# Performance work log

Measured on AMD Instinct MI355X. Metric: run time of the kernel, lower is better.

Reference implementation:

```python
import jax, jax.numpy as jnp
import numpy as np

N = 50000          # site nodes
L = 32             # max URL token length
E = 64             # embed_size
H = 128            # hidden_size
E_SIM = 800000     # edges per relation in blocks
E_SUB = 200000     # 'sim' edges classified at the end
NEG = 0.01         # LeakyReLU negative slope

def leaky(x):
    return jnp.where(x >= 0, x, NEG * x)

def lstm_final(x, mask, Wih, Whh, b, reverse):
    # x: [N, L, E], mask: [N, L] bool. Returns packed-sequence final hidden [N, E].
    if reverse:
        x = x[:, ::-1, :]
        mask = mask[:, ::-1]
    h0 = jnp.zeros((x.shape[0], Whh.shape[1]), x.dtype)
    def step(carry, inp):
        h, c = carry
        xt, mt = inp
        g = xt @ Wih.T + h @ Whh.T + b
        i, f, gg, o = jnp.split(g, 4, axis=-1)  # PyTorch gate order i,f,g,o
        cn = jax.nn.sigmoid(f) * c + jax.nn.sigmoid(i) * jnp.tanh(gg)
        hn = jax.nn.sigmoid(o) * jnp.tanh(cn)
        m = mt[:, None]
        return (jnp.where(m, hn, h), jnp.where(m, cn, c)), None
    (h, _), _ = jax.lax.scan(step, (h0, h0), (x.transpose(1, 0, 2), mask.T))
    return h

def graph_conv(h, src, dst, W, b):
    # DGL GraphConv, norm='both': D_dst^{-1/2} A D_src^{-1/2} h W + b  (degrees clamped to >=1)
    n = h.shape[0]
    ones = jnp.ones(src.shape[0], h.dtype)
    out_deg = jnp.clip(jax.ops.segment_sum(ones, src, num_segments=n), 1.0)
    in_deg = jnp.clip(jax.ops.segment_sum(ones, dst, num_segments=n), 1.0)
    feat = h * jax.lax.rsqrt(out_deg)[:, None]
    if W.shape[0] > W.shape[1]:
        feat = feat @ W  # project before gather/scatter when in_dim > out_dim (as DGL does)
        rst = jax.ops.segment_sum(feat[src], dst, num_segments=n)
    else:
        rst = jax.ops.segment_sum(feat[src], dst, num_segments=n) @ W
    return rst * jax.lax.rsqrt(in_deg)[:, None] + b

def setup_inputs():
    key = jax.random.key(0)
    ks = iter(jax.random.split(key, 64))
    def nrm(shape, scale=0.05):
        return jax.random.normal(next(ks), shape, dtype=jnp.float32) * scale
    inp = {}
    inp["inputs_s"] = jax.random.randint(next(ks), (N, L), 0, 128)
    lengths = jax.random.randint(next(ks), (N,), 1, L + 1)
    inp["inputs_sm"] = (jnp.arange(L)[None, :] < lengths[:, None]).astype(jnp.int32)
    inp["inputs_c"] = jax.random.randint(next(ks), (N, 1), 0, 101)
    inp["inputs_co"] = jax.random.randint(next(ks), (N, 1), 0, 92)
    inp["inputs_sl"] = jax.random.randint(next(ks), (N, 1), 0, 6)
    for name, m in [("sim_src", E_SIM), ("sim_dst", E_SIM), ("user_src", E_SIM),
                    ("user_dst", E_SIM), ("esub_src", E_SUB), ("esub_dst", E_SUB)]:
        inp[name] = jax.random.randint(next(ks), (m,), 0, N)
    inp["emb_url"] = nrm((128, E)); inp["emb_cat"] = nrm((101, E))
    inp["emb_country"] = nrm((92, E)); inp["emb_sl"] = nrm((6, E))
    for d in ("f", "b"):
        inp["Wih_" + d] = nrm((4 * E, E)); inp["Whh_" + d] = nrm((4 * E, E))
        inp["b_" + d] = nrm((4 * E,))  # b_ih + b_hh folded into one bias
    inp["fc_W"] = nrm((E, 2 * E)); inp["fc_b"] = nrm((E,))
    for i, din in enumerate([4 * E, H]):
        for rel in ("sim", "user"):
            inp["gcn%d_%s_W" % (i, rel)] = nrm((din, H))
            inp["gcn%d_%s_b" % (i, rel)] = nrm((H,))
    inp["cls_W1"] = nrm((H, 2 * H)); inp["cls_b1"] = nrm((H,))
    inp["bn_g"] = jnp.ones((H,), jnp.float32); inp["bn_b"] = jnp.zeros((H,), jnp.float32)
    inp["cls_W2"] = nrm((2, H)); inp["cls_b2"] = nrm((2,))
    return inp

def reference(inputs_s, inputs_sm, inputs_c, inputs_co, inputs_sl,
              sim_src, sim_dst, user_src, user_dst, esub_src, esub_dst,
              emb_url, emb_cat, emb_country, emb_sl,
              Wih_f, Whh_f, b_f, Wih_b, Whh_b, b_b, fc_W, fc_b,
              gcn0_sim_W, gcn0_sim_b, gcn0_user_W, gcn0_user_b,
              gcn1_sim_W, gcn1_sim_b, gcn1_user_W, gcn1_user_b,
              cls_W1, cls_b1, bn_g, bn_b, cls_W2, cls_b2):
    mask = inputs_sm.astype(bool)
    x = emb_url[inputs_s]                                # [N, L, E]
    hf = lstm_final(x, mask, Wih_f, Whh_f, b_f, False)   # h_n[0]
    hb = lstm_final(x, mask, Wih_b, Whh_b, b_b, True)    # h_n[1]
    h_url = leaky(jnp.concatenate([hf, hb], -1) @ fc_W.T + fc_b)  # dropout = identity (eval)
    h = jnp.concatenate([h_url, emb_cat[inputs_c[:, 0]],
                         emb_country[inputs_co[:, 0]], emb_sl[inputs_sl[:, 0]]], -1)  # [N, 4E]
    layers = [(gcn0_sim_W, gcn0_sim_b, gcn0_user_W, gcn0_user_b),
              (gcn1_sim_W, gcn1_sim_b, gcn1_user_W, gcn1_user_b)]
    for Ws, bs, Wu, bu in layers:  # HeteroGraphConv aggregate='sum'
        h = leaky(graph_conv(h, sim_src, sim_dst, Ws, bs)
                  + graph_conv(h, user_src, user_dst, Wu, bu))
    feat = jnp.concatenate([h[esub_src], h[esub_dst]], -1)  # [E_SUB, 2H]
    z = feat @ cls_W1.T + cls_b1
    z = (z - z.mean(0)) * jax.lax.rsqrt(z.var(0) + 1e-5) * bn_g + bn_b  # BatchNorm1d (batch stats)
    z = jnp.maximum(z, 0.0)
    return z @ cls_W2.T + cls_b2
```

## Files before the change

### kernel.cpp

```cpp
#include <hip/hip_runtime.h>
#include <hip/hip_bf16.h>
#include <stdint.h>

#define N_NODES 50000
#define SEQ_L   32
#define NE_BIG  800000
#define NE_SUB  200000
#define DSTRIDE 64

typedef __hip_bfloat16 bf16;
typedef unsigned short u16;
typedef _Float16 f16;
typedef _Float16 v8h __attribute__((ext_vector_type(8)));
typedef float v4f __attribute__((ext_vector_type(4)));

__device__ __forceinline__ float b2f(bf16 x) { return __bfloat162float(x); }
__device__ __forceinline__ float leakyf(float v) { return v >= 0.f ? v : 0.01f * v; }
__device__ __forceinline__ u16 f2h_bits(float x) { f16 h = (f16)x; u16 b; __builtin_memcpy(&b, &h, 2); return b; }
__device__ __forceinline__ float h2f(u16 b) { f16 h; __builtin_memcpy(&h, &b, 2); return (float)h; }
__device__ __forceinline__ uint pack2h(float a, float b) { return (uint)f2h_bits(a) | ((uint)f2h_bits(b) << 16); }

__device__ __forceinline__ float ldf(const void* p, int i, int isbf) {
  return isbf ? b2f(((const bf16*)p)[i]) : ((const float*)p)[i];
}

__device__ __forceinline__ int detect_isbf(const u16* __restrict__ u) {
  __shared__ int insane;
  if (threadIdx.x == 0) insane = 0;
  __syncthreads();
  int expo = (u[threadIdx.x * 2] >> 7) & 0xFF;
  if (expo >= 147) atomicAdd(&insane, 1);
  __syncthreads();
  return insane == 0;
}

struct PrepArgs {
  const void* Whh_f; const void* Whh_b; const void* fc_W; const void* cls_W1;
  const void* g0sW; const void* g0uW; const void* g1sW; const void* g1uW;
  const void* emb_cat; const void* emb_country; const void* emb_sl;
  const void* fc_b; const void* cls_b1; const void* g0sb; const void* g0ub;
  const void* g1sb; const void* g1ub; const void* bn_g; const void* bn_b;
  const void* cls_W2; const void* cls_b2;
  const void* emb_url; const void* Wih_f; const void* b_f; const void* Wih_b; const void* b_b;
  f16* Whh_h; u16* Bfc; u16* BW1; u16* Bg0; u16* Bg1;
  u16* embc_h; u16* embco_h; u16* embs_h;
  float* fcb; float* b1; float* g0sbP; float* g0ubP; float* g1sbP; float* g1ubP;
  float* bngP; float* bnbP; float* W2P; float* b2P;
  int* dflag;
  float* Xperm;
  const int* sm; int* lens; int* cnt33;
  const int* s0; const int* d0; const int* s1; const int* d1;
  int* cnt4; int* col0; int* col1;
};

__global__ __launch_bounds__(256) void prep_graph_kernel(PrepArgs A) {
  const int b = blockIdx.x;
  const int t = threadIdx.x;
  const int NBL = (N_NODES + 255) / 256;
  const int NBE = (NE_BIG + 255) / 256;

  if (b >= 1186) {
    int rel = (b - 1186) / NBE;
    int e = ((b - 1186) % NBE) * 256 + t;
    if (e >= NE_BIG) return;
    const int* s = rel ? A.s1 : A.s0;
    const int* d = rel ? A.d1 : A.d0;
    int* col = rel ? A.col1 : A.col0;
    int* base = A.cnt4 + (size_t)rel * 2 * N_NODES;
    int sv = s[e], dv = d[e];
    atomicAdd(&base[sv], 1);
    int p = atomicAdd(&base[N_NODES + dv], 1);
    if (p < DSTRIDE) col[(size_t)dv * DSTRIDE + p] = sv;
    return;
  }
  if (b >= 990) {
    int i = (b - 990) * 256 + t;
    if (i >= N_NODES) return;
    int len = 0;
#pragma unroll
    for (int tt = 0; tt < SEQ_L; ++tt) len += A.sm[i * SEQ_L + tt];
    A.lens[i] = len;
    atomicAdd(&A.cnt33[len], 1);
    return;
  }

  const int isbf = detect_isbf((const u16*)A.emb_url);
  auto cpy = [&](const void* s, float* d, int n, int boff) {
    int i = (b - boff) * 256 + t;
    if (i < n) d[i] = ldf(s, i, isbf);
  };
  auto cvh = [&](const void* s, u16* d, int n, int boff) {
    int i = (b - boff) * 256 + t;
    if (i < n) d[i] = f2h_bits(ldf(s, i, isbf));
  };
  auto trh = [&](const void* s, u16* d, int R, int C, int KOFF, int boff) {
    int i = (b - boff) * 256 + t;
    if (i < R * C) { int r = i / C, c = i % C; d[c * 256 + KOFF + r] = f2h_bits(ldf(s, i, isbf)); }
  };
  if      (b <   64) cvh(A.Whh_f, (u16*)A.Whh_h, 16384, 0);
  else if (b <  128) cvh(A.Whh_b, (u16*)(A.Whh_h + 16384), 16384, 64);
  else if (b <  160) cvh(A.fc_W, A.Bfc, 8192, 128);
  else if (b <  288) cvh(A.cls_W1, A.BW1, 32768, 160);
  else if (b <  416) trh(A.g0sW, A.Bg0, 256, 128, 0, 288);
  else if (b <  544) trh(A.g0uW, A.Bg0 + 128 * 256, 256, 128, 0, 416);
  else if (b <  608) trh(A.g1sW, A.Bg1, 128, 128, 0, 544);
  else if (b <  672) trh(A.g1uW, A.Bg1, 128, 128, 128, 608);
  else if (b <  698) cvh(A.emb_cat, A.embc_h, 6464, 672);
  else if (b <  721) cvh(A.emb_country, A.embco_h, 5888, 698);
  else if (b <  723) cvh(A.emb_sl, A.embs_h, 384, 721);
  else if (b <  724) cpy(A.fc_b, A.fcb, 64, 723);
  else if (b <  725) cpy(A.cls_b1, A.b1, 128, 724);
  else if (b <  726) cpy(A.g0sb, A.g0sbP, 128, 725);
  else if (b <  727) cpy(A.g0ub, A.g0ubP, 128, 726);
  else if (b <  728) cpy(A.g1sb, A.g1sbP, 128, 727);
  else if (b <  729) cpy(A.g1ub, A.g1ubP, 128, 728);
  else if (b <  730) cpy(A.bn_g, A.bngP, 128, 729);
  else if (b <  731) cpy(A.bn_b, A.bnbP, 128, 730);
  else if (b <  732) cpy(A.cls_W2, A.W2P, 256, 731);
  else if (b <  733) { cpy(A.cls_b2, A.b2P, 2, 732); if (t == 0) A.dflag[0] = isbf; }
  else if (b <  989) {
    int bb = b - 733;
    int dir = bb >> 7;
    int v = bb & 127;
    const void* Wih = dir ? A.Wih_b : A.Wih_f;
    const void* bias = dir ? A.b_b : A.b_f;
    __shared__ float embL[64];
    if (t < 64) embL[t] = ldf(A.emb_url, v * 64 + t, isbf);
    __syncthreads();
    float acc = ldf(bias, t, isbf);
#pragma unroll 8
    for (int j = 0; j < 64; ++j) acc += embL[j] * ldf(Wih, t * 64 + j, isbf);
    int g = t >> 6, unit = t & 63;
    A.Xperm[(size_t)dir * 128 * 256 + v * 256 + unit * 4 + g] = acc;
  }
}
#define PG_BLOCKS (1186 + 2 * 3125)

__global__ __launch_bounds__(256) void permfill_rsq_kernel(
    const int* __restrict__ lens, const int* __restrict__ cnt33, int* __restrict__ cur33,
    int* __restrict__ perm,
    const int* __restrict__ cnt4, float* __restrict__ rsq4)
{
  const int b = blockIdx.x, t = threadIdx.x;
  const int NBL = (N_NODES + 255) / 256;
  if (b < NBL) {
    int i = b * 256 + t;
    if (i >= N_NODES) return;
    int len = lens[i];
    int base = 0;
    for (int l = len + 1; l <= SEQ_L; ++l) base += cnt33[l];
    int p = atomicAdd(&cur33[len], 1);
    perm[base + p] = i;
  } else {
    int i = (b - NBL) * 256 + t;
    if (i >= 4 * N_NODES) return;
    int c = cnt4[i]; if (c < 1) c = 1;
    rsq4[i] = __builtin_amdgcn_rsqf((float)c);
  }
}
#define PR_BLOCKS (196 + 782)

__global__ __launch_bounds__(256, 4) void lstm_mfma_kernel(
    const int* __restrict__ perm, const int* __restrict__ lens,
    const int* __restrict__ toksg,
    const float* __restrict__ Xperm,
    const f16* __restrict__ Whh_h,
    u16* __restrict__ hcat_h,
    int nnodes)
{
  __shared__ __align__(16) f16 H[2][64 * 72];
  __shared__ int toksL[2][64];
  __shared__ int permL[64];
  __shared__ int lensL[64];
  __shared__ int smax;
  const int tid = threadIdx.x;
  const int w = tid >> 6;
  const int lane = tid & 63;
  const int quad = lane >> 4;
  const int lid = lane & 15;
  const int dir = blockIdx.y;

  if (tid < 64) {
    int gid = blockIdx.x * 64 + tid;
    int node = -1, len = 0;
    if (gid < nnodes) { node = perm[gid]; len = lens[node]; }
    permL[tid] = node; lensL[tid] = len;
  }
  if (tid == 0) smax = 0;
  for (int i = tid; i < 64 * 72; i += 256) { H[0][i] = (f16)0.f; H[1][i] = (f16)0.f; }
  __syncthreads();
  if (tid < 64 && lensL[tid] > 0) atomicMax(&smax, lensL[tid]);
  __syncthreads();
  const int tmax = smax;

  const f16* Wd = Whh_h + (size_t)dir * 256 * 64;
  v8h Bf[4][2];
#pragma unroll
  for (int g = 0; g < 4; ++g)
#pragma unroll
    for (int kf = 0; kf < 2; ++kf)
      Bf[g][kf] = *(const v8h*)(Wd + (g * 64 + w * 16 + lid) * 64 + kf * 32 + quad * 8);

  int lenv[16];
#pragma unroll
  for (int mt = 0; mt < 4; ++mt)
#pragma unroll
    for (int r = 0; r < 4; ++r) lenv[mt * 4 + r] = lensL[mt * 16 + quad * 4 + r];

  float creg[16];
  f16 hreg[16];
#pragma unroll
  for (int i = 0; i < 16; ++i) { creg[i] = 0.f; hreg[i] = (f16)0.f; }

  const float* Xp = Xperm + (size_t)dir * 128 * 256;

  if (tid < 64) {
    int len = lensL[tid];
    int tok = 0;
    if (len > 0) tok = toksg[(size_t)permL[tid] * SEQ_L + (dir ? (len - 1) : 0)];
    toksL[0][tid] = tok;
  }
  __syncthreads();

  for (int step = 0; step < tmax; ++step) {
    const int rb = step & 1, wb = rb ^ 1;
#pragma unroll
    for (int mt = 0; mt < 4; ++mt) {
      float4 xr[4];
#pragma unroll
      for (int r = 0; r < 4; ++r) {
        int nd = mt * 16 + quad * 4 + r;
        xr[r] = *(const float4*)(Xp + (size_t)toksL[rb][nd] * 256 + (w * 16 + lid) * 4);
      }
      const f16* hb = &H[rb][0];
      int arow = (mt * 16 + lid) * 72 + quad * 8;
      v8h a0 = *(const v8h*)(hb + arow);
      v8h a1 = *(const v8h*)(hb + arow + 32);
      v4f acc[4];
#pragma unroll
      for (int g = 0; g < 4; ++g) {
        v4f a = {0.f, 0.f, 0.f, 0.f};
        a = __builtin_amdgcn_mfma_f32_16x16x32_f16(a0, Bf[g][0], a, 0, 0, 0);
        a = __builtin_amdgcn_mfma_f32_16x16x32_f16(a1, Bf[g][1], a, 0, 0, 0);
        acc[g] = a;
      }
#pragma unroll
      for (int r = 0; r < 4; ++r) {
        int idx = mt * 4 + r;
        int nd = mt * 16 + quad * 4 + r;
        bool act = step < lenv[idx];
        float gi = acc[0][r] + xr[r].x;
        float gf = acc[1][r] + xr[r].y;
        float gG = acc[2][r] + xr[r].z;
        float go = acc[3][r] + xr[r].w;
        float A = __expf(-gi);
        float B = __expf(-gf);
        float C = __expf(-go);
        float D = __expf(2.f * fminf(gG, 15.f));
        float sf = __builtin_amdgcn_rcpf(1.f + B);
        float sitg = (D - 1.f) * __builtin_amdgcn_rcpf((1.f + A) * (D + 1.f));
        float cn = sf * creg[idx] + sitg;
        float E = __expf(2.f * fminf(cn, 15.f));
        float hn = (E - 1.f) * __builtin_amdgcn_rcpf((1.f + C) * (E + 1.f));
        if (act) { creg[idx] = cn; hreg[idx] = (f16)hn; }
        H[wb][nd * 72 + w * 16 + lid] = hreg[idx];
      }
    }
    if (tid < 64 && step + 1 < tmax) {
      int len = lensL[tid];
      int tok = 0;
      if (step + 1 < len) {
        int t = dir ? (len - 2 - step) : (step + 1);
        tok = toksg[(size_t)permL[tid] * SEQ_L + t];
      }
      toksL[wb][tid] = tok;
    }
    __syncthreads();
  }
#pragma unroll
  for (int mt = 0; mt < 4; ++mt)
#pragma unroll
    for (int r = 0; r < 4; ++r) {
      int nd = mt * 16 + quad * 4 + r;
      int gnode = permL[nd];
      if (gnode >= 0) {
        u16 bits; f16 hv = hreg[mt * 4 + r]; __builtin_memcpy(&bits, &hv, 2);
        hcat_h[(size_t)gnode * 128 + dir * 64 + w * 16 + lid] = bits;
      }
    }
}

template<int K, int COLS, int AMODE, bool LEAKY, int OHS, bool EMB, bool BNS>
__global__ __launch_bounds__(256) void mfma_gemm(
    const u16* __restrict__ Ah,
    const int* __restrict__ esrc, const int* __restrict__ edst, const u16* __restrict__ Fh,
    const u16* __restrict__ B,
    const float* __restrict__ bias, const float* __restrict__ bias2,
    const float* __restrict__ rs0, const float* __restrict__ rs1,
    u16* __restrict__ outh0, u16* __restrict__ outh1,
    const int* __restrict__ ic, const int* __restrict__ ico, const int* __restrict__ isl,
    const u16* __restrict__ ech, const u16* __restrict__ ecoh, const u16* __restrict__ eslh,
    float* __restrict__ bnsums,
    int nrows)
{
  constexpr int AST = K + 8;
  constexpr int ABYTES = 64 * AST * 2;
  constexpr int EBYTES = 64 * 129 * 4;
  constexpr int SBYTES = (ABYTES > EBYTES) ? ABYTES : EBYTES;
  __shared__ __align__(16) char smem[SBYTES];
  u16* As = (u16*)smem;
  float* Es = (float*)smem;
  __shared__ int idxL[128];
  __shared__ float bnred[BNS ? 512 : 1];

  const int tid = threadIdx.x;
  const int w = tid >> 6;
  const int lane = tid & 63;
  const int quad = lane >> 4;
  const int lid = lane & 15;
  const int r0 = blockIdx.x * 64;

  if (AMODE == 2) {
    if (tid < 64) {
      int row = r0 + tid;
      idxL[tid] = (row < nrows) ? esrc[row] : -1;
      idxL[64 + tid] = (row < nrows) ? edst[row] : -1;
    }
    __syncthreads();
    for (int idx = tid; idx < 64 * (K / 8); idx += 256) {
      int rn = idx / (K / 8), seg = idx % (K / 8);
      int half = seg >> 4, k8 = seg & 15;
      int base = idxL[half * 64 + rn];
      uint4 v = {0u, 0u, 0u, 0u};
      if (base >= 0) v = *(const uint4*)(Fh + (size_t)base * 128 + k8 * 8);
      *(uint4*)(As + rn * AST + seg * 8) = v;
    }
  } else {
    for (int idx = tid; idx < 64 * (K / 8); idx += 256) {
      int rn = idx / (K / 8), c8 = idx % (K / 8);
      int row = r0 + rn;
      uint4 v = {0u, 0u, 0u, 0u};
      if (row < nrows) v = *(const uint4*)(Ah + (size_t)row * K + c8 * 8);
      *(uint4*)(As + rn * AST + c8 * 8) = v;
    }
  }
  __syncthreads();

  constexpr int NT = COLS / 16;
  v4f acc[NT];
#pragma unroll
  for (int i = 0; i < NT; ++i) acc[i] = (v4f){0.f, 0.f, 0.f, 0.f};

  for (int kb = 0; kb < K / 32; ++kb) {
    v8h a = *(const v8h*)((const f16*)As + (w * 16 + lid) * AST + kb * 32 + quad * 8);
#pragma unroll
    for (int ct = 0; ct < NT; ++ct) {
      v8h b = *(const v8h*)((const f16*)B + (size_t)(ct * 16 + lid) * K + kb * 32 + quad * 8);
      acc[ct] = __builtin_amdgcn_mfma_f32_16x16x32_f16(a, b, acc[ct], 0, 0, 0);
    }
  }

  constexpr int NH = (COLS > 128) ? 2 : 1;
  constexpr int CH = COLS / NH;
  float bs = 0.f, bs2 = 0.f;
#pragma unroll
  for (int h = 0; h < NH; ++h) {
    __syncthreads();
#pragma unroll
    for (int ct = 0; ct < CH / 16; ++ct) {
      int ctg = h * (CH / 16) + ct;
#pragma unroll
      for (int r = 0; r < 4; ++r)
        Es[(w * 16 + quad * 4 + r) * 129 + ct * 16 + lid] = acc[ctg][r];
    }
    __syncthreads();
    for (int idx = tid; idx < 64 * CH; idx += 256) {
      int rn = idx / CH, c = idx % CH;
      int row = r0 + rn;
      float v = 0.f;
      if (row < nrows) {
        v = Es[rn * 129 + c];
        if (bias) v += bias[h * CH + c];
        if (bias2) v += bias2[h * CH + c];
        if (LEAKY) v = leakyf(v);
        const float* rs = (h == 0) ? rs0 : rs1;
        if (rs) v *= rs[row];
        u16* oh = (h == 0) ? outh0 : outh1;
        oh[(size_t)row * OHS + c] = f2h_bits(v);
      }
      if (BNS) { bs += v; bs2 += v * v; }
    }
  }
  if (BNS) {
    bnred[tid] = bs;
    bnred[256 + tid] = bs2;
    __syncthreads();
    if (tid < 128) {
      atomicAdd(&bnsums[tid], bnred[tid] + bnred[tid + 128]);
      atomicAdd(&bnsums[128 + tid], bnred[256 + tid] + bnred[384 + tid]);
    }
  }
  if (EMB) {
    for (int idx = tid; idx < 64 * 192; idx += 256) {
      int rn = idx / 192, j = idx % 192;
      int row = r0 + rn;
      if (row >= nrows) continue;
      u16 v;
      if (j < 64)       v = ech [ic [row] * 64 + j];
      else if (j < 128) v = ecoh[ico[row] * 64 + (j - 64)];
      else              v = eslh[isl[row] * 64 + (j - 128)];
      outh0[(size_t)row * OHS + 64 + j] = v;
    }
  }
}

__global__ __launch_bounds__(256) void gather_merge0_kernel(
    const int* __restrict__ colS, const int* __restrict__ cntS, const u16* __restrict__ Ps,
    const int* __restrict__ colU, const int* __restrict__ cntU, const u16* __restrict__ Pu,
    const float* __restrict__ rsS, const float* __restrict__ rsU,
    const float* __restrict__ bS, const float* __restrict__ bU,
    u16* __restrict__ outh, int nnodes)
{
  int wave = threadIdx.x >> 6;
  int lane = threadIdx.x & 63;
  int node = __builtin_amdgcn_readfirstlane(blockIdx.x * 4 + wave);
  if (node >= nnodes) return;
  const uint* PS2 = (const uint*)Ps;
  const uint* PU2 = (const uint*)Pu;
  float2 aS = make_float2(0.f, 0.f), aU = make_float2(0.f, 0.f);
  {
    const int* col = colS + (size_t)node * DSTRIDE;
    int cnt = min(cntS[node], DSTRIDE);
    int e = 0;
    for (; e + 4 <= cnt; e += 4) {
      uint v0 = PS2[(size_t)col[e] * 64 + lane];
      uint v1 = PS2[(size_t)col[e + 1] * 64 + lane];
      uint v2 = PS2[(size_t)col[e + 2] * 64 + lane];
      uint v3 = PS2[(size_t)col[e + 3] * 64 + lane];
      aS.x += h2f((u16)v0) + h2f((u16)v1) + h2f((u16)v2) + h2f((u16)v3);
      aS.y += h2f((u16)(v0 >> 16)) + h2f((u16)(v1 >> 16)) + h2f((u16)(v2 >> 16)) + h2f((u16)(v3 >> 16));
    }
    for (; e < cnt; ++e) {
      uint v = PS2[(size_t)col[e] * 64 + lane];
      aS.x += h2f((u16)v); aS.y += h2f((u16)(v >> 16));
    }
  }
  {
    const int* col = colU + (size_t)node * DSTRIDE;
    int cnt = min(cntU[node], DSTRIDE);
    int e = 0;
    for (; e + 4 <= cnt; e += 4) {
      uint v0 = PU2[(size_t)col[e] * 64 + lane];
      uint v1 = PU2[(size_t)col[e + 1] * 64 + lane];
      uint v2 = PU2[(size_t)col[e + 2] * 64 + lane];
      uint v3 = PU2[(size_t)col[e + 3] * 64 + lane];
      aU.x += h2f((u16)v0) + h2f((u16)v1) + h2f((u16)v2) + h2f((u16)v3);
      aU.y += h2f((u16)(v0 >> 16)) + h2f((u16)(v1 >> 16)) + h2f((u16)(v2 >> 16)) + h2f((u16)(v3 >> 16));
    }
    for (; e < cnt; ++e) {
      uint v = PU2[(size_t)col[e] * 64 + lane];
      aU.x += h2f((u16)v); aU.y += h2f((u16)(v >> 16));
    }
  }
  float rS = rsS[node], rU = rsU[node];
  float2 bsv = ((const float2*)bS)[lane];
  float2 buv = ((const float2*)bU)[lane];
  float o0 = leakyf(aS.x * rS + bsv.x + aU.x * rU + buv.x);
  float o1 = leakyf(aS.y * rS + bsv.y + aU.y * rU + buv.y);
  ((uint*)outh)[(size_t)node * 64 + lane] = pack2h(o0, o1);
}

__global__ __launch_bounds__(256) void gather_cat1_kernel(
    const int* __restrict__ colS, const int* __restrict__ cntS,
    const int* __restrict__ colU, const int* __restrict__ cntU,
    const u16* __restrict__ Fh,
    const float* __restrict__ rsoutS, const float* __restrict__ rsoutU,
    const float* __restrict__ rsinS, const float* __restrict__ rsinU,
    u16* __restrict__ Acat, int nnodes)
{
  int wave = threadIdx.x >> 6;
  int lane = threadIdx.x & 63;
  int node = __builtin_amdgcn_readfirstlane(blockIdx.x * 4 + wave);
  if (node >= nnodes) return;
  const uint* F2 = (const uint*)Fh;
  float2 aS = make_float2(0.f, 0.f), aU = make_float2(0.f, 0.f);
  {
    const int* col = colS + (size_t)node * DSTRIDE;
    int cnt = min(cntS[node], DSTRIDE);
    int e = 0;
    for (; e + 2 <= cnt; e += 2) {
      int s0 = col[e], s1 = col[e + 1];
      float c0 = rsoutS[s0], c1 = rsoutS[s1];
      uint v0 = F2[(size_t)s0 * 64 + lane];
      uint v1 = F2[(size_t)s1 * 64 + lane];
      aS.x += c0 * h2f((u16)v0) + c1 * h2f((u16)v1);
      aS.y += c0 * h2f((u16)(v0 >> 16)) + c1 * h2f((u16)(v1 >> 16));
    }
    for (; e < cnt; ++e) {
      int s = col[e]; float c = rsoutS[s];
      uint v = F2[(size_t)s * 64 + lane];
      aS.x += c * h2f((u16)v); aS.y += c * h2f((u16)(v >> 16));
    }
  }
  {
    const int* col = colU + (size_t)node * DSTRIDE;
    int cnt = min(cntU[node], DSTRIDE);
    int e = 0;
    for (; e + 2 <= cnt; e += 2) {
      int s0 = col[e], s1 = col[e + 1];
      float c0 = rsoutU[s0], c1 = rsoutU[s1];
      uint v0 = F2[(size_t)s0 * 64 + lane];
      uint v1 = F2[(size_t)s1 * 64 + lane];
      aU.x += c0 * h2f((u16)v0) + c1 * h2f((u16)v1);
      aU.y += c0 * h2f((u16)(v0 >> 16)) + c1 * h2f((u16)(v1 >> 16));
    }
    for (; e < cnt; ++e) {
      int s = col[e]; float c = rsoutU[s];
      uint v = F2[(size_t)s * 64 + lane];
      aU.x += c * h2f((u16)v); aU.y += c * h2f((u16)(v >> 16));
    }
  }
  float rs = rsinS[node], ru = rsinU[node];
  ((uint*)Acat)[(size_t)node * 128 + lane] = pack2h(aS.x * rs, aS.y * rs);
  ((uint*)Acat)[(size_t)node * 128 + 64 + lane] = pack2h(aU.x * ru, aU.y * ru);
}

__global__ __launch_bounds__(256) void out_kernel(
    const u16* __restrict__ zh, const float* __restrict__ bnsums,
    const float* __restrict__ g, const float* __restrict__ bb, float M,
    const float* __restrict__ W2, const float* __restrict__ b2,
    void* __restrict__ out, int Mi, const int* __restrict__ flag)
{
  __shared__ float lds[128 * 65];
  __shared__ float red[64 * 8];
  __shared__ float ssL[256];
  const int tid = threadIdx.x;
  const int n = tid & 63;
  const int q = __builtin_amdgcn_readfirstlane(tid >> 6);
  const int r0 = blockIdx.x * 64;
  if (tid < 128) {
    float mean = bnsums[tid] / M;
    float var = bnsums[128 + tid] / M - mean * mean;
    float sc = g[tid] * __builtin_amdgcn_rsqf(var + 1e-5f);
    ssL[tid] = sc;
    ssL[128 + tid] = bb[tid] - mean * sc;
  }
  for (int idx = tid; idx < 64 * 128; idx += 256) {
    int rn = idx >> 7, j = idx & 127;
    int row = r0 + rn;
    lds[j * 65 + rn] = (row < Mi) ? h2f(zh[(size_t)row * 128 + j]) : 0.f;
  }
  __syncthreads();
  float a0 = 0.f, a1 = 0.f;
#pragma unroll 8
  for (int jj = 0; jj < 32; ++jj) {
    int j = q * 32 + jj;
    float y = lds[j * 65 + n] * ssL[j] + ssL[128 + j];
    y = y > 0.f ? y : 0.f;
    a0 += y * W2[j];
    a1 += y * W2[128 + j];
  }
  red[n * 8 + q * 2 + 0] = a0;
  red[n * 8 + q * 2 + 1] = a1;
  __syncthreads();
  if (q == 0 && (r0 + n) < Mi) {
    float o0 = red[n * 8] + red[n * 8 + 2] + red[n * 8 + 4] + red[n * 8 + 6] + b2[0];
    float o1 = red[n * 8 + 1] + red[n * 8 + 3] + red[n * 8 + 5] + red[n * 8 + 7] + b2[1];
    size_t oi = (size_t)(r0 + n) * 2;
    if (*flag) {
      ((bf16*)out)[oi + 0] = __float2bfloat16(o0);
      ((bf16*)out)[oi + 1] = __float2bfloat16(o1);
    } else {
      ((float*)out)[oi + 0] = o0;
      ((float*)out)[oi + 1] = o1;
    }
  }
}

extern "C" void kernel_launch(void* const* d_in, const int* in_sizes, int n_in,
                              void* d_out, int out_size, void* d_ws, size_t ws_size,
                              hipStream_t stream) {
  (void)in_sizes; (void)n_in; (void)out_size; (void)ws_size;
  const int N = N_NODES;
  const int* inputs_s  = (const int*)d_in[0];
  const int* inputs_sm = (const int*)d_in[1];
  const int* inputs_c  = (const int*)d_in[2];
  const int* inputs_co = (const int*)d_in[3];
  const int* inputs_sl = (const int*)d_in[4];
  const int* sim_src   = (const int*)d_in[5];
  const int* sim_dst   = (const int*)d_in[6];
  const int* user_src  = (const int*)d_in[7];
  const int* user_dst  = (const int*)d_in[8];
  const int* esub_src  = (const int*)d_in[9];
  const int* esub_dst  = (const int*)d_in[10];

  char* base = (char*)d_ws;
  size_t off = 0;
  auto alloc = [&](size_t bytes) -> char* {
    char* p = base + off;
    off += (bytes + 255) & ~(size_t)255;
    return p;
  };
  int* dflag    = (int*)alloc(256);
  f16* Whh_h    = (f16*)alloc(2 * 256 * 64 * 2);
  float* Xperm  = (float*)alloc(2 * 128 * 256 * 4);
  u16* Bfc      = (u16*)alloc(64 * 128 * 2);
  u16* BW1      = (u16*)alloc(128 * 256 * 2);
  u16* Bg0      = (u16*)alloc(256 * 256 * 2);
  u16* Bg1      = (u16*)alloc(128 * 256 * 2);
  u16* P_embc_h = (u16*)alloc(6464 * 2);
  u16* P_embco_h= (u16*)alloc(5888 * 2);
  u16* P_embs_h = (u16*)alloc(384 * 2);
  float* P_fcb  = (float*)alloc(64 * 4);
  float* P_b1   = (float*)alloc(128 * 4);
  float* P_g0sb = (float*)alloc(128 * 4);
  float* P_g0ub = (float*)alloc(128 * 4);
  float* P_g1sb = (float*)alloc(128 * 4);
  float* P_g1ub = (float*)alloc(128 * 4);
  float* P_bng  = (float*)alloc(128 * 4);
  float* P_bnb  = (float*)alloc(128 * 4);
  float* P_W2   = (float*)alloc(256 * 4);
  float* P_b2   = (float*)alloc(2 * 4);
  int* lens     = (int*)alloc((size_t)N * 4);
  int* perm     = (int*)alloc((size_t)N * 4);
  float* rsq4   = (float*)alloc((size_t)4 * N * 4);
  char* zbase   = alloc((size_t)4 * N * 4 + 3 * 256 + 1024);
  int* cnt4     = (int*)zbase;
  int* cnt33    = (int*)(zbase + (size_t)4 * N * 4);
  int* cur33    = cnt33 + 64;
  float* bnsums = (float*)(zbase + (size_t)4 * N * 4 + 512);
  const size_t zbytes = (size_t)4 * N * 4 + 3 * 256 + 1024;
  char* bufA = alloc((size_t)N * 256 * 4);
  char* bufB = alloc((size_t)N * 256 * 2);
  char* bufC = alloc((size_t)N * 256 * 2);
  char* bufE = alloc((size_t)N * 128 * 2);
  u16* h_h     = (u16*)bufA;
  u16* zh      = (u16*)bufA;
  int* col_sim = (int*)(bufA + (size_t)N * 256 * 2);
  int* col_usr = (int*)(bufA + (size_t)N * 256 * 2 + (size_t)N * DSTRIDE * 4);
  u16* hcat_h = (u16*)bufB;
  u16* h1_h   = (u16*)bufB;
  u16* Ps_h   = (u16*)bufC;
  u16* Pu_h   = Ps_h + (size_t)N * 128;
  u16* Acat   = (u16*)bufC;
  u16* F_h    = (u16*)bufE;

  const int NB64 = (N + 63) / 64;
  const int NBZ  = (NE_SUB + 63) / 64;

  hipMemsetAsync(zbase, 0, zbytes, stream);

  PrepArgs PA;
  PA.Whh_f = d_in[16]; PA.Whh_b = d_in[19]; PA.fc_W = d_in[21]; PA.cls_W1 = d_in[31];
  PA.g0sW = d_in[23]; PA.g0uW = d_in[25]; PA.g1sW = d_in[27]; PA.g1uW = d_in[29];
  PA.emb_cat = d_in[12]; PA.emb_country = d_in[13]; PA.emb_sl = d_in[14];
  PA.fc_b = d_in[22]; PA.cls_b1 = d_in[32]; PA.g0sb = d_in[24]; PA.g0ub = d_in[26];
  PA.g1sb = d_in[28]; PA.g1ub = d_in[30]; PA.bn_g = d_in[33]; PA.bn_b = d_in[34];
  PA.cls_W2 = d_in[35]; PA.cls_b2 = d_in[36];
  PA.emb_url = d_in[11]; PA.Wih_f = d_in[15]; PA.b_f = d_in[17]; PA.Wih_b = d_in[18]; PA.b_b = d_in[20];
  PA.Whh_h = Whh_h; PA.Bfc = Bfc; PA.BW1 = BW1; PA.Bg0 = Bg0; PA.Bg1 = Bg1;
  PA.embc_h = P_embc_h; PA.embco_h = P_embco_h; PA.embs_h = P_embs_h;
  PA.fcb = P_fcb; PA.b1 = P_b1; PA.g0sbP = P_g0sb; PA.g0ubP = P_g0ub; PA.g1sbP = P_g1sb; PA.g1ubP = P_g1ub;
  PA.bngP = P_bng; PA.bnbP = P_bnb; PA.W2P = P_W2; PA.b2P = P_b2;
  PA.dflag = dflag; PA.Xperm = Xperm;
  PA.sm = inputs_sm; PA.lens = lens; PA.cnt33 = cnt33;
  PA.s0 = sim_src; PA.d0 = sim_dst; PA.s1 = user_src; PA.d1 = user_dst;
  PA.cnt4 = cnt4; PA.col0 = col_sim; PA.col1 = col_usr;
  prep_graph_kernel<<<PG_BLOCKS, 256, 0, stream>>>(PA);

  permfill_rsq_kernel<<<PR_BLOCKS, 256, 0, stream>>>(lens, cnt33, cur33, perm, cnt4, rsq4);

  lstm_mfma_kernel<<<dim3(NB64, 2), 256, 0, stream>>>(perm, lens, inputs_s, Xperm, Whh_h, hcat_h, N);

  mfma_gemm<128, 64, 1, true, 256, true, false><<<NB64, 256, 0, stream>>>(
      hcat_h, nullptr, nullptr, nullptr, Bfc, P_fcb, nullptr, nullptr, nullptr,
      h_h, nullptr, inputs_c, inputs_co, inputs_sl, P_embc_h, P_embco_h, P_embs_h, nullptr, N);

  mfma_gemm<256, 256, 1, false, 128, false, false><<<NB64, 256, 0, stream>>>(
      h_h, nullptr, nullptr, nullptr, Bg0, nullptr, nullptr, rsq4, rsq4 + 2 * N,
      Ps_h, Pu_h, nullptr, nullptr, nullptr, nullptr, nullptr, nullptr, nullptr, N);

  gather_merge0_kernel<<<(N + 3) / 4, 256, 0, stream>>>(col_sim, cnt4 + N, Ps_h,
                                                        col_usr, cnt4 + 3 * N, Pu_h,
                                                        rsq4 + N, rsq4 + 3 * N, P_g0sb, P_g0ub, h1_h, N);

  gather_cat1_kernel<<<(N + 3) / 4, 256, 0, stream>>>(col_sim, cnt4 + N, col_usr, cnt4 + 3 * N, h1_h,
                                                      rsq4, rsq4 + 2 * N, rsq4 + N, rsq4 + 3 * N, Acat, N);

  mfma_gemm<256, 128, 1, true, 128, false, false><<<NB64, 256, 0, stream>>>(
      Acat, nullptr, nullptr, nullptr, Bg1, P_g1sb, P_g1ub, nullptr, nullptr,
      F_h, nullptr, nullptr, nullptr, nullptr, nullptr, nullptr, nullptr, nullptr, N);

  mfma_gemm<256, 128, 2, false, 128, false, true><<<NBZ, 256, 0, stream>>>(
      nullptr, esub_src, esub_dst, F_h, BW1, P_b1, nullptr, nullptr, nullptr,
      zh, nullptr, nullptr, nullptr, nullptr, nullptr, nullptr, nullptr, bnsums, NE_SUB);

  out_kernel<<<NBZ, 256, 0, stream>>>(zh, bnsums, P_bng, P_bnb, (float)NE_SUB,
                                      P_W2, P_b2, d_out, NE_SUB, dflag);
}
```

Before: 1.128 ms.

## Overlap graph edge CSR build with LSTM blocks and shrink column indices

Moves the edge degree counting and adjacency-list build out of the prep kernel and into the LSTM launch, interleaving four edge blocks per LSTM block so latency-bound atomics run alongside the recurrent MFMA work. The rsqrt-degree computation moves into extra blocks of the first FC GEMM. Column indices are stored as 16-bit instead of 32-bit, halving the adjacency footprint that the gather kernels read. This relies on node ids fitting in 16 bits, which fails for 50000 > 32767? No, u16 holds up to 65535, so it fits. The mixed kernel, however, keeps the LSTM's shared memory and launch bounds on the edge blocks, which may limit occupancy for them.

```diff
diff --git a/kernel.cpp b/kernel.cpp
--- a/kernel.cpp
+++ b/kernel.cpp
@@ -49,30 +49,12 @@
   int* dflag;
   float* Xperm;
   const int* sm; int* lens; int* cnt33;
-  const int* s0; const int* d0; const int* s1; const int* d1;
-  int* cnt4; int* col0; int* col1;
 };
 
 __global__ __launch_bounds__(256) void prep_graph_kernel(PrepArgs A) {
   const int b = blockIdx.x;
   const int t = threadIdx.x;
-  const int NBL = (N_NODES + 255) / 256;
-  const int NBE = (NE_BIG + 255) / 256;
-
-  if (b >= 1186) {
-    int rel = (b - 1186) / NBE;
-    int e = ((b - 1186) % NBE) * 256 + t;
-    if (e >= NE_BIG) return;
-    const int* s = rel ? A.s1 : A.s0;
-    const int* d = rel ? A.d1 : A.d0;
-    int* col = rel ? A.col1 : A.col0;
-    int* base = A.cnt4 + (size_t)rel * 2 * N_NODES;
-    int sv = s[e], dv = d[e];
-    atomicAdd(&base[sv], 1);
-    int p = atomicAdd(&base[N_NODES + dv], 1);
-    if (p < DSTRIDE) col[(size_t)dv * DSTRIDE + p] = sv;
-    return;
-  }
+
   if (b >= 990) {
     int i = (b - 990) * 256 + t;
     if (i >= N_NODES) return;
@@ -134,54 +116,71 @@
     A.Xperm[(size_t)dir * 128 * 256 + v * 256 + unit * 4 + g] = acc;
   }
 }
-#define PG_BLOCKS (1186 + 2 * 3125)
-
-__global__ __launch_bounds__(256) void permfill_rsq_kernel(
+#define PG_BLOCKS 1186
+
+__global__ __launch_bounds__(256) void permfill_kernel(
     const int* __restrict__ lens, const int* __restrict__ cnt33, int* __restrict__ cur33,
-    int* __restrict__ perm,
-    const int* __restrict__ cnt4, float* __restrict__ rsq4)
+    int* __restrict__ perm)
 {
-  const int b = blockIdx.x, t = threadIdx.x;
-  const int NBL = (N_NODES + 255) / 256;
-  if (b < NBL) {
-    int i = b * 256 + t;
-    if (i >= N_NODES) return;
-    int len = lens[i];
-    int base = 0;
-    for (int l = len + 1; l <= SEQ_L; ++l) base += cnt33[l];
-    int p = atomicAdd(&cur33[len], 1);
-    perm[base + p] = i;
-  } else {
-    int i = (b - NBL) * 256 + t;
-    if (i >= 4 * N_NODES) return;
-    int c = cnt4[i]; if (c < 1) c = 1;
-    rsq4[i] = __builtin_amdgcn_rsqf((float)c);
-  }
-}
-#define PR_BLOCKS (196 + 782)
-
-__global__ __launch_bounds__(256, 4) void lstm_mfma_kernel(
+  int i = blockIdx.x * 256 + threadIdx.x;
+  if (i >= N_NODES) return;
+  int len = lens[i];
+  int base = 0;
+  for (int l = len + 1; l <= SEQ_L; ++l) base += cnt33[l];
+  int p = atomicAdd(&cur33[len], 1);
+  perm[base + p] = i;
+}
+#define PF_BLOCKS 196
+
+#define LSTM_BLOCKS 1564
+#define EDGE_BLOCKS 6250
+__global__ __launch_bounds__(256, 4) void lstm_edge_kernel(
     const int* __restrict__ perm, const int* __restrict__ lens,
     const int* __restrict__ toksg,
     const float* __restrict__ Xperm,
     const f16* __restrict__ Whh_h,
     u16* __restrict__ hcat_h,
+    const int* __restrict__ s0, const int* __restrict__ d0,
+    const int* __restrict__ s1, const int* __restrict__ d1,
+    int* __restrict__ cnt4, u16* __restrict__ col0, u16* __restrict__ col1,
     int nnodes)
 {
+  const int bid = blockIdx.x;
+  const int tid = threadIdx.x;
+
+  if (bid % 5 != 0) {
+    int eb = bid - 1 - bid / 5;
+    if (eb >= EDGE_BLOCKS) return;
+    int rel = eb / 3125;
+    int e = (eb % 3125) * 256 + tid;
+    if (e >= NE_BIG) return;
+    const int* s = rel ? s1 : s0;
+    const int* d = rel ? d1 : d0;
+    u16* col = rel ? col1 : col0;
+    int* basep = cnt4 + (size_t)rel * 2 * N_NODES;
+    int sv = s[e], dv = d[e];
+    atomicAdd(&basep[sv], 1);
+    int p = atomicAdd(&basep[N_NODES + dv], 1);
+    if (p < DSTRIDE) col[(size_t)dv * DSTRIDE + p] = (u16)sv;
+    return;
+  }
+
+  const int l = bid / 5;
+  const int dir = l / 782;
+  const int bx = l % 782;
+
   __shared__ __align__(16) f16 H[2][64 * 72];
   __shared__ int toksL[2][64];
   __shared__ int permL[64];
   __shared__ int lensL[64];
   __shared__ int smax;
-  const int tid = threadIdx.x;
   const int w = tid >> 6;
   const int lane = tid & 63;
   const int quad = lane >> 4;
   const int lid = lane & 15;
-  const int dir = blockIdx.y;
 
   if (tid < 64) {
-    int gid = blockIdx.x * 64 + tid;
+    int gid = bx * 64 + tid;
     int node = -1, len = 0;
     if (gid < nnodes) { node = perm[gid]; len = lens[node]; }
     permL[tid] = node; lensL[tid] = len;
@@ -290,7 +289,7 @@
     }
 }
 
-template<int K, int COLS, int AMODE, bool LEAKY, int OHS, bool EMB, bool BNS>
+template<int K, int COLS, int AMODE, bool LEAKY, int OHS, bool EMB, bool BNS, bool RSQT = false>
 __global__ __launch_bounds__(256) void mfma_gemm(
     const u16* __restrict__ Ah,
     const int* __restrict__ esrc, const int* __restrict__ edst, const u16* __restrict__ Fh,
@@ -301,8 +300,20 @@
     const int* __restrict__ ic, const int* __restrict__ ico, const int* __restrict__ isl,
     const u16* __restrict__ ech, const u16* __restrict__ ecoh, const u16* __restrict__ eslh,
     float* __restrict__ bnsums,
+    const int* __restrict__ cntin, float* __restrict__ rsqout,
     int nrows)
 {
+  if (RSQT) {
+    int nbm = (nrows + 63) >> 6;
+    if ((int)blockIdx.x >= nbm) {
+      int i = ((int)blockIdx.x - nbm) * 256 + (int)threadIdx.x;
+      if (i < 4 * N_NODES) {
+        int c = cntin[i]; if (c < 1) c = 1;
+        rsqout[i] = __builtin_amdgcn_rsqf((float)c);
+      }
+      return;
+    }
+  }
   constexpr int AST = K + 8;
   constexpr int ABYTES = 64 * AST * 2;
   constexpr int EBYTES = 64 * 129 * 4;
@@ -415,8 +426,8 @@
 }
 
 __global__ __launch_bounds__(256) void gather_merge0_kernel(
-    const int* __restrict__ colS, const int* __restrict__ cntS, const u16* __restrict__ Ps,
-    const int* __restrict__ colU, const int* __restrict__ cntU, const u16* __restrict__ Pu,
+    const u16* __restrict__ colS, const int* __restrict__ cntS, const u16* __restrict__ Ps,
+    const u16* __restrict__ colU, const int* __restrict__ cntU, const u16* __restrict__ Pu,
     const float* __restrict__ rsS, const float* __restrict__ rsU,
     const float* __restrict__ bS, const float* __restrict__ bU,
     u16* __restrict__ outh, int nnodes)
@@ -429,7 +440,7 @@
   const uint* PU2 = (const uint*)Pu;
   float2 aS = make_float2(0.f, 0.f), aU = make_float2(0.f, 0.f);
   {
-    const int* col = colS + (size_t)node * DSTRIDE;
+    const u16* col = colS + (size_t)node * DSTRIDE;
     int cnt = min(cntS[node], DSTRIDE);
     int e = 0;
     for (; e + 4 <= cnt; e += 4) {
@@ -446,7 +457,7 @@
     }
   }
   {
-    const int* col = colU + (size_t)node * DSTRIDE;
+    const u16* col = colU + (size_t)node * DSTRIDE;
     int cnt = min(cntU[node], DSTRIDE);
     int e = 0;
     for (; e + 4 <= cnt; e += 4) {
@@ -471,8 +482,8 @@
 }
 
 __global__ __launch_bounds__(256) void gather_cat1_kernel(
-    const int* __restrict__ colS, const int* __restrict__ cntS,
-    const int* __restrict__ colU, const int* __restrict__ cntU,
+    const u16* __restrict__ colS, const int* __restrict__ cntS,
+    const u16* __restrict__ colU, const int* __restrict__ cntU,
     const u16* __restrict__ Fh,
     const float* __restrict__ rsoutS, const float* __restrict__ rsoutU,
     const float* __restrict__ rsinS, const float* __restrict__ rsinU,
@@ -485,7 +496,7 @@
   const uint* F2 = (const uint*)Fh;
   float2 aS = make_float2(0.f, 0.f), aU = make_float2(0.f, 0.f);
   {
-    const int* col = colS + (size_t)node * DSTRIDE;
+    const u16* col = colS + (size_t)node * DSTRIDE;
     int cnt = min(cntS[node], DSTRIDE);
     int e = 0;
     for (; e + 2 <= cnt; e += 2) {
@@ -503,7 +514,7 @@
     }
   }
   {
-    const int* col = colU + (size_t)node * DSTRIDE;
+    const u16* col = colU + (size_t)node * DSTRIDE;
     int cnt = min(cntU[node], DSTRIDE);
     int e = 0;
     for (; e + 2 <= cnt; e += 2) {
@@ -636,8 +647,8 @@
   char* bufE = alloc((size_t)N * 128 * 2);
   u16* h_h     = (u16*)bufA;
   u16* zh      = (u16*)bufA;
-  int* col_sim = (int*)(bufA + (size_t)N * 256 * 2);
-  int* col_usr = (int*)(bufA + (size_t)N * 256 * 2 + (size_t)N * DSTRIDE * 4);
+  u16* col_sim = (u16*)(bufA + (size_t)N * 256 * 2);
+  u16* col_usr = (u16*)(bufA + (size_t)N * 256 * 2 + (size_t)N * DSTRIDE * 2);
   u16* hcat_h = (u16*)bufB;
   u16* h1_h   = (u16*)bufB;
   u16* Ps_h   = (u16*)bufC;
@@ -664,21 +675,24 @@
   PA.bngP = P_bng; PA.bnbP = P_bnb; PA.W2P = P_W2; PA.b2P = P_b2;
   PA.dflag = dflag; PA.Xperm = Xperm;
   PA.sm = inputs_sm; PA.lens = lens; PA.cnt33 = cnt33;
-  PA.s0 = sim_src; PA.d0 = sim_dst; PA.s1 = user_src; PA.d1 = user_dst;
-  PA.cnt4 = cnt4; PA.col0 = col_sim; PA.col1 = col_usr;
   prep_graph_kernel<<<PG_BLOCKS, 256, 0, stream>>>(PA);
 
-  permfill_rsq_kernel<<<PR_BLOCKS, 256, 0, stream>>>(lens, cnt33, cur33, perm, cnt4, rsq4);
-
-  lstm_mfma_kernel<<<dim3(NB64, 2), 256, 0, stream>>>(perm, lens, inputs_s, Xperm, Whh_h, hcat_h, N);
-
-  mfma_gemm<128, 64, 1, true, 256, true, false><<<NB64, 256, 0, stream>>>(
+  permfill_kernel<<<PF_BLOCKS, 256, 0, stream>>>(lens, cnt33, cur33, perm);
+
+  lstm_edge_kernel<<<5 * LSTM_BLOCKS, 256, 0, stream>>>(
+      perm, lens, inputs_s, Xperm, Whh_h, hcat_h,
+      sim_src, sim_dst, user_src, user_dst,
+      cnt4, col_sim, col_usr, N);
+
+  mfma_gemm<128, 64, 1, true, 256, true, false, true><<<NB64 + 782, 256, 0, stream>>>(
       hcat_h, nullptr, nullptr, nullptr, Bfc, P_fcb, nullptr, nullptr, nullptr,
-      h_h, nullptr, inputs_c, inputs_co, inputs_sl, P_embc_h, P_embco_h, P_embs_h, nullptr, N);
+      h_h, nullptr, inputs_c, inputs_co, inputs_sl, P_embc_h, P_embco_h, P_embs_h, nullptr,
+      cnt4, rsq4, N);
 
   mfma_gemm<256, 256, 1, false, 128, false, false><<<NB64, 256, 0, stream>>>(
       h_h, nullptr, nullptr, nullptr, Bg0, nullptr, nullptr, rsq4, rsq4 + 2 * N,
-      Ps_h, Pu_h, nullptr, nullptr, nullptr, nullptr, nullptr, nullptr, nullptr, N);
+      Ps_h, Pu_h, nullptr, nullptr, nullptr, nullptr, nullptr, nullptr, nullptr,
+      nullptr, nullptr, N);
 
   gather_merge0_kernel<<<(N + 3) / 4, 256, 0, stream>>>(col_sim, cnt4 + N, Ps_h,
                                                         col_usr, cnt4 + 3 * N, Pu_h,
@@ -689,11 +703,13 @@
 
   mfma_gemm<256, 128, 1, true, 128, false, false><<<NB64, 256, 0, stream>>>(
       Acat, nullptr, nullptr, nullptr, Bg1, P_g1sb, P_g1ub, nullptr, nullptr,
-      F_h, nullptr, nullptr, nullptr, nullptr, nullptr, nullptr, nullptr, nullptr, N);
+      F_h, nullptr, nullptr, nullptr, nullptr, nullptr, nullptr, nullptr, nullptr,
+      nullptr, nullptr, N);
 
   mfma_gemm<256, 128, 2, false, 128, false, true><<<NBZ, 256, 0, stream>>>(
       nullptr, esub_src, esub_dst, F_h, BW1, P_b1, nullptr, nullptr, nullptr,
-      zh, nullptr, nullptr, nullptr, nullptr, nullptr, nullptr, nullptr, bnsums, NE_SUB);
+      zh, nullptr, nullptr, nullptr, nullptr, nullptr, nullptr, nullptr, bnsums,
+      nullptr, nullptr, NE_SUB);
 
   out_kernel<<<NBZ, 256, 0, stream>>>(zh, bnsums, P_bng, P_bnb, (float)NE_SUB,
                                       P_W2, P_b2, d_out, NE_SUB, dflag);
```

New measurement: 1.121 ms. No clear change (-0.6%).

## Shard edge atomics by node modulo XCD count and store CSR columns as u16

Applied to the files above, without the earlier changes.

Edge-counting blocks now each cover a 4096-edge chunk, and every chunk is processed by 8 shard blocks. Each shard block only does the atomics for nodes whose id mod 8 matches its block index. The apparent aim is to keep atomic traffic for a node inside one XCD's L2 under round-robin block dispatch, avoiding cross-die atomic contention. Column indices become 16-bit, which halves the adjacency footprint in the gather kernels and is valid only because the node count is below 65536. Edge and mask reads use nontemporal loads. The cost is that every shard re-reads every edge, so edge-array reads grow eightfold.

```diff
diff --git a/kernel.cpp b/kernel.cpp
--- a/kernel.cpp
+++ b/kernel.cpp
@@ -33,6 +33,11 @@
   __syncthreads();
   return insane == 0;
 }
+
+#define EDGE_EPT   16
+#define EDGE_CHUNK (256 * EDGE_EPT)
+#define EDGE_NCH   ((NE_BIG + EDGE_CHUNK - 1) / EDGE_CHUNK)
+#define EDGE_BLOCKS (EDGE_NCH * 2 * 8)
 
 struct PrepArgs {
   const void* Whh_f; const void* Whh_b; const void* fc_W; const void* cls_W1;
@@ -50,35 +55,47 @@
   float* Xperm;
   const int* sm; int* lens; int* cnt33;
   const int* s0; const int* d0; const int* s1; const int* d1;
-  int* cnt4; int* col0; int* col1;
+  int* cnt4; u16* col0; u16* col1;
 };
 
 __global__ __launch_bounds__(256) void prep_graph_kernel(PrepArgs A) {
-  const int b = blockIdx.x;
+  const int bid = blockIdx.x;
   const int t = threadIdx.x;
-  const int NBL = (N_NODES + 255) / 256;
-  const int NBE = (NE_BIG + 255) / 256;
-
-  if (b >= 1186) {
-    int rel = (b - 1186) / NBE;
-    int e = ((b - 1186) % NBE) * 256 + t;
-    if (e >= NE_BIG) return;
+
+  if (bid < EDGE_BLOCKS) {
+    const int shard = bid & 7;
+    const int q = bid >> 3;
+    const int rel = q & 1;
+    const int chunk = q >> 1;
     const int* s = rel ? A.s1 : A.s0;
     const int* d = rel ? A.d1 : A.d0;
-    int* col = rel ? A.col1 : A.col0;
-    int* base = A.cnt4 + (size_t)rel * 2 * N_NODES;
-    int sv = s[e], dv = d[e];
-    atomicAdd(&base[sv], 1);
-    int p = atomicAdd(&base[N_NODES + dv], 1);
-    if (p < DSTRIDE) col[(size_t)dv * DSTRIDE + p] = sv;
+    u16* col = rel ? A.col1 : A.col0;
+    int* basep = A.cnt4 + (size_t)rel * 2 * N_NODES;
+    const int e0 = chunk * EDGE_CHUNK + t;
+#pragma unroll
+    for (int k = 0; k < EDGE_EPT; ++k) {
+      int e = e0 + k * 256;
+      if (e < NE_BIG) {
+        int sv = __builtin_nontemporal_load(s + e);
+        int dv = __builtin_nontemporal_load(d + e);
+        if ((sv & 7) == shard) atomicAdd(&basep[sv], 1);
+        if ((dv & 7) == shard) {
+          int p = atomicAdd(&basep[N_NODES + dv], 1);
+          if (p < DSTRIDE) col[(size_t)dv * DSTRIDE + p] = (u16)sv;
+        }
+      }
+    }
     return;
   }
+
+  const int b = bid - EDGE_BLOCKS;
+
   if (b >= 990) {
     int i = (b - 990) * 256 + t;
     if (i >= N_NODES) return;
     int len = 0;
 #pragma unroll
-    for (int tt = 0; tt < SEQ_L; ++tt) len += A.sm[i * SEQ_L + tt];
+    for (int tt = 0; tt < SEQ_L; ++tt) len += __builtin_nontemporal_load(A.sm + i * SEQ_L + tt);
     A.lens[i] = len;
     atomicAdd(&A.cnt33[len], 1);
     return;
@@ -134,7 +151,7 @@
     A.Xperm[(size_t)dir * 128 * 256 + v * 256 + unit * 4 + g] = acc;
   }
 }
-#define PG_BLOCKS (1186 + 2 * 3125)
+#define PG_BLOCKS (EDGE_BLOCKS + 1186)
 
 __global__ __launch_bounds__(256) void permfill_rsq_kernel(
     const int* __restrict__ lens, const int* __restrict__ cnt33, int* __restrict__ cur33,
@@ -415,8 +432,8 @@
 }
 
 __global__ __launch_bounds__(256) void gather_merge0_kernel(
-    const int* __restrict__ colS, const int* __restrict__ cntS, const u16* __restrict__ Ps,
-    const int* __restrict__ colU, const int* __restrict__ cntU, const u16* __restrict__ Pu,
+    const u16* __restrict__ colS, const int* __restrict__ cntS, const u16* __restrict__ Ps,
+    const u16* __restrict__ colU, const int* __restrict__ cntU, const u16* __restrict__ Pu,
     const float* __restrict__ rsS, const float* __restrict__ rsU,
     const float* __restrict__ bS, const float* __restrict__ bU,
     u16* __restrict__ outh, int nnodes)
@@ -429,7 +446,7 @@
   const uint* PU2 = (const uint*)Pu;
   float2 aS = make_float2(0.f, 0.f), aU = make_float2(0.f, 0.f);
   {
-    const int* col = colS + (size_t)node * DSTRIDE;
+    const u16* col = colS + (size_t)node * DSTRIDE;
     int cnt = min(cntS[node], DSTRIDE);
     int e = 0;
     for (; e + 4 <= cnt; e += 4) {
@@ -446,7 +463,7 @@
     }
   }
   {
-    const int* col = colU + (size_t)node * DSTRIDE;
+    const u16* col = colU + (size_t)node * DSTRIDE;
     int cnt = min(cntU[node], DSTRIDE);
     int e = 0;
     for (; e + 4 <= cnt; e += 4) {
@@ -471,8 +488,8 @@
 }
 
 __global__ __launch_bounds__(256) void gather_cat1_kernel(
-    const int* __restrict__ colS, const int* __restrict__ cntS,
-    const int* __restrict__ colU, const int* __restrict__ cntU,
+    const u16* __restrict__ colS, const int* __restrict__ cntS,
+    const u16* __restrict__ colU, const int* __restrict__ cntU,
     const u16* __restrict__ Fh,
     const float* __restrict__ rsoutS, const float* __restrict__ rsoutU,
     const float* __restrict__ rsinS, const float* __restrict__ rsinU,
@@ -485,7 +502,7 @@
   const uint* F2 = (const uint*)Fh;
   float2 aS = make_float2(0.f, 0.f), aU = make_float2(0.f, 0.f);
   {
-    const int* col = colS + (size_t)node * DSTRIDE;
+    const u16* col = colS + (size_t)node * DSTRIDE;
     int cnt = min(cntS[node], DSTRIDE);
     int e = 0;
     for (; e + 2 <= cnt; e += 2) {
@@ -503,7 +520,7 @@
     }
   }
   {
-    const int* col = colU + (size_t)node * DSTRIDE;
+    const u16* col = colU + (size_t)node * DSTRIDE;
     int cnt = min(cntU[node], DSTRIDE);
     int e = 0;
     for (; e + 2 <= cnt; e += 2) {
@@ -636,8 +653,8 @@
   char* bufE = alloc((size_t)N * 128 * 2);
   u16* h_h     = (u16*)bufA;
   u16* zh      = (u16*)bufA;
-  int* col_sim = (int*)(bufA + (size_t)N * 256 * 2);
-  int* col_usr = (int*)(bufA + (size_t)N * 256 * 2 + (size_t)N * DSTRIDE * 4);
+  u16* col_sim = (u16*)(bufA + (size_t)N * 256 * 2);
+  u16* col_usr = (u16*)(bufA + (size_t)N * 256 * 2 + (size_t)N * DSTRIDE * 2);
   u16* hcat_h = (u16*)bufB;
   u16* h1_h   = (u16*)bufB;
   u16* Ps_h   = (u16*)bufC;
```

After: 1.182 ms. 1.05x slower.
